# Kernel optimization log

Measured on AMD Instinct MI355X. Metric: run time of the kernel, lower is better.

Reference implementation:

```python
import jax, jax.numpy as jnp
import numpy as np

B, D, L, H = 512, 512, 32, 300  # batch, input_dim, latent_dim, hidden_dim


def setup_inputs() -> dict:
    key = jax.random.key(0)
    ks = jax.random.split(key, 16)
    s = lambda k, *sh: jax.random.normal(k, sh, dtype=jnp.float32) * 0.05
    return {
        "x": jax.random.normal(ks[0], (B, D), dtype=jnp.float32),
        "eps": jax.random.normal(ks[1], (B, L), dtype=jnp.float32),
        "W": jax.random.normal(ks[2], (D, L), dtype=jnp.float32),  # mask (get_generator_mask -> W)
        "qz_w1": s(ks[3], D, H), "qz_b1": s(ks[4], H),
        "qz_w2": s(ks[5], H, H), "qz_b2": s(ks[6], H),
        "zm_w": s(ks[7], H, L), "zm_b": s(ks[8], L),
        "zl_w": s(ks[9], H, L), "zl_b": s(ks[10], L),
        "gen_w1": s(ks[11], L, H),               # no bias (bias=False)
        "gen_w2": s(ks[12], H, H), "gen_b2": s(ks[13], H),
        "col_w": s(ks[14], D, H), "col_b": s(ks[15], D),  # stacked column_means Linears
    }


def reference(x, eps, W, qz_w1, qz_b1, qz_w2, qz_b2, zm_w, zm_b, zl_w, zl_b,
              gen_w1, gen_w2, gen_b2, col_w, col_b):
    # encode
    h = jax.nn.relu(x @ qz_w1 + qz_b1)
    h = jax.nn.relu(h @ qz_w2 + qz_b2)
    z_mean = h @ zm_w + zm_b
    z_log_var = h @ zl_w + zl_b
    # reparameterize (eps supplied as input)
    z = z_mean + eps * jnp.exp(0.5 * z_log_var)
    # decode: per-column masked generator MLP, batched over columns j
    masked = W[:, None, :] * z[None, :, :]                 # [D, B, L]
    g = jax.nn.relu(jnp.einsum('jbl,lh->jbh', masked, gen_w1))
    g = jax.nn.relu(jnp.einsum('jbh,hk->jbk', g, gen_w2) + gen_b2)
    x_rec = jnp.einsum('jbh,jh->jb', g, col_w) + col_b[:, None]  # [D, B]
    x_mean = x_rec.T                                       # [B, D]
    return (x_mean, z, z_mean, z_log_var)
```

## Files before the change

### kernel.cpp

```cpp
#include <hip/hip_runtime.h>

#define B_ 512
#define D_ 512
#define L_ 32
#define H_ 300
#define NT 19
#define NS 10
#define G1S 308

typedef unsigned short ushort_t;
typedef __bf16 bf16x8 __attribute__((ext_vector_type(8)));
typedef float f32x4 __attribute__((ext_vector_type(4)));

__device__ __forceinline__ float bf2f(unsigned int hi16) {
    return __uint_as_float(hi16 << 16);
}
__device__ __forceinline__ ushort_t f2bf(float f) {
    unsigned int u = __float_as_uint(f);
    u += 0x7fffu + ((u >> 16) & 1u);
    return (ushort_t)(u >> 16);
}

union B8 { ushort_t u[8]; uint4 q; bf16x8 v; uint2 d[2]; };

__global__ __launch_bounds__(64) void prep_kernel(
        const float* __restrict__ gw1, const float* __restrict__ gw2,
        const float* __restrict__ qw1, const float* __restrict__ qw2,
        const float* __restrict__ zmw, const float* __restrict__ zlw,
        ushort_t* __restrict__ gw1f, ushort_t* __restrict__ gw2f,
        ushort_t* __restrict__ w1hi, ushort_t* __restrict__ w1lo,
        ushort_t* __restrict__ w2hi, ushort_t* __restrict__ w2lo,
        ushort_t* __restrict__ w3hi, ushort_t* __restrict__ w3lo) {
    int blk = blockIdx.x;
    int l = threadIdx.x, grp = l >> 4, li = l & 15;
    if (blk < 209) {
        const float* src; int K, nt, s; ushort_t* dst;
        if (blk < 19) { nt = blk; s = 0; src = gw1; K = 32; dst = gw1f + (nt * 64 + l) * 8; }
        else { int i = blk - 19; nt = i / 10; s = i % 10; src = gw2; K = 300;
               dst = gw2f + ((nt * 10 + s) * 64 + l) * 8; }
        int n = nt * 16 + li;
        B8 V;
        #pragma unroll
        for (int i = 0; i < 8; ++i) {
            int k = 32 * s + 8 * grp + i;
            V.u[i] = f2bf((k < K && n < H_) ? src[k * H_ + n] : 0.f);
        }
        *reinterpret_cast<uint4*>(dst) = V.q;
    } else {
        const float* src = nullptr; int K, N, nt, s, stacked = 0;
        ushort_t *dh, *dl;
        if (blk < 513)      { int i = blk - 209; nt = i / 16; s = i % 16; src = qw1; K = 512; N = 300;
                              dh = w1hi + ((nt * 16 + s) * 64 + l) * 8; dl = w1lo + ((nt * 16 + s) * 64 + l) * 8; }
        else if (blk < 703) { int i = blk - 513; nt = i / 10; s = i % 10; src = qw2; K = 300; N = 300;
                              dh = w2hi + ((nt * 10 + s) * 64 + l) * 8; dl = w2lo + ((nt * 10 + s) * 64 + l) * 8; }
        else                { int i = blk - 703; nt = i / 10; s = i % 10; K = 300; N = 64; stacked = 1;
                              dh = w3hi + ((nt * 10 + s) * 64 + l) * 8; dl = w3lo + ((nt * 10 + s) * 64 + l) * 8; }
        int n = nt * 16 + li;
        B8 Vh, Vl;
        #pragma unroll
        for (int i = 0; i < 8; ++i) {
            int k = 32 * s + 8 * grp + i;
            float v = 0.f;
            if (k < K && n < N) {
                if (!stacked) v = src[k * N + n];
                else          v = (n < 32) ? zmw[k * 32 + n] : zlw[k * 32 + (n - 32)];
            }
            ushort_t h = f2bf(v);
            Vh.u[i] = h;
            Vl.u[i] = f2bf(v - bf2f(h));
        }
        *reinterpret_cast<uint4*>(dh) = Vh.q;
        *reinterpret_cast<uint4*>(dl) = Vl.q;
    }
}

template<int KSTEPS, bool RELU>
__global__ __launch_bounds__(256) void enc_gemm_f32(const float* __restrict__ A, int lda,
        const ushort_t* __restrict__ Whi, const ushort_t* __restrict__ Wlo,
        const float* __restrict__ bias, float* __restrict__ out, int ldo,
        int Ncols, int ntiles) {
    const int tid = threadIdx.x;
    const int w = tid >> 6, lane = tid & 63;
    const int grp = lane >> 4, li = lane & 15;
    const int r0 = blockIdx.x * 16;
    const int nt = blockIdx.y * 4 + w;
    const bool active = nt < ntiles;

    f32x4 acc = {0.f, 0.f, 0.f, 0.f};
    for (int s = 0; s < KSTEPS; ++s) {
        int kb = 32 * s + 8 * grp;
        B8 Ah, Al;
        if (kb + 8 <= lda) {
            const float* ap = A + (size_t)(r0 + li) * lda + kb;
            float4 f0 = *reinterpret_cast<const float4*>(ap);
            float4 f1 = *reinterpret_cast<const float4*>(ap + 4);
            float fv[8] = {f0.x, f0.y, f0.z, f0.w, f1.x, f1.y, f1.z, f1.w};
            #pragma unroll
            for (int i = 0; i < 8; ++i) {
                ushort_t h = f2bf(fv[i]);
                Ah.u[i] = h;
                Al.u[i] = f2bf(fv[i] - bf2f(h));
            }
        } else {
            Ah.q = make_uint4(0, 0, 0, 0);
            Al.q = make_uint4(0, 0, 0, 0);
        }
        if (active) {
            bf16x8 bh = *reinterpret_cast<const bf16x8*>(
                Whi + ((size_t)(nt * KSTEPS + s) * 64 + lane) * 8);
            bf16x8 bl = *reinterpret_cast<const bf16x8*>(
                Wlo + ((size_t)(nt * KSTEPS + s) * 64 + lane) * 8);
            acc = __builtin_amdgcn_mfma_f32_16x16x32_bf16(Ah.v, bh, acc, 0, 0, 0);
            acc = __builtin_amdgcn_mfma_f32_16x16x32_bf16(Al.v, bh, acc, 0, 0, 0);
            acc = __builtin_amdgcn_mfma_f32_16x16x32_bf16(Ah.v, bl, acc, 0, 0, 0);
        }
    }
    if (active) {
        int h = nt * 16 + li;
        float bv = (bias != nullptr && h < Ncols) ? bias[h] : 0.f;
        #pragma unroll
        for (int r = 0; r < 4; ++r) {
            float v = acc[r] + bv;
            if (RELU) v = fmaxf(v, 0.f);
            if (h >= Ncols) v = 0.f;
            out[(size_t)(r0 + 4 * grp + r) * ldo + h] = v;
        }
    }
}

__global__ __launch_bounds__(256) void enc3_reparam(const float* __restrict__ h2,
        const ushort_t* __restrict__ w3hi, const ushort_t* __restrict__ w3lo,
        const float* __restrict__ zmb, const float* __restrict__ zlb,
        const float* __restrict__ eps, float* __restrict__ out, float* __restrict__ zb) {
    __shared__ float zs[16][64];
    const int tid = threadIdx.x;
    const int w = tid >> 6, lane = tid & 63;
    const int grp = lane >> 4, li = lane & 15;
    const int r0 = blockIdx.x * 16;

    f32x4 acc = {0.f, 0.f, 0.f, 0.f};
    for (int s = 0; s < 10; ++s) {
        int kb = 32 * s + 8 * grp;
        B8 Ah, Al;
        if (kb + 8 <= 304) {
            const float* ap = h2 + (size_t)(r0 + li) * 304 + kb;
            float4 f0 = *reinterpret_cast<const float4*>(ap);
            float4 f1 = *reinterpret_cast<const float4*>(ap + 4);
            float fv[8] = {f0.x, f0.y, f0.z, f0.w, f1.x, f1.y, f1.z, f1.w};
            #pragma unroll
            for (int i = 0; i < 8; ++i) {
                ushort_t h = f2bf(fv[i]);
                Ah.u[i] = h;
                Al.u[i] = f2bf(fv[i] - bf2f(h));
            }
        } else {
            Ah.q = make_uint4(0, 0, 0, 0);
            Al.q = make_uint4(0, 0, 0, 0);
        }
        bf16x8 bh = *reinterpret_cast<const bf16x8*>(w3hi + ((size_t)(w * 10 + s) * 64 + lane) * 8);
        bf16x8 bl = *reinterpret_cast<const bf16x8*>(w3lo + ((size_t)(w * 10 + s) * 64 + lane) * 8);
        acc = __builtin_amdgcn_mfma_f32_16x16x32_bf16(Ah.v, bh, acc, 0, 0, 0);
        acc = __builtin_amdgcn_mfma_f32_16x16x32_bf16(Al.v, bh, acc, 0, 0, 0);
        acc = __builtin_amdgcn_mfma_f32_16x16x32_bf16(Ah.v, bl, acc, 0, 0, 0);
    }
    #pragma unroll
    for (int r = 0; r < 4; ++r) zs[4 * grp + r][w * 16 + li] = acc[r];
    __syncthreads();

    for (int idx = tid; idx < 512; idx += 256) {
        int m = idx >> 5, l2 = idx & 31;
        int row = r0 + m;
        float zm = zs[m][l2] + zmb[l2];
        float zl = zs[m][32 + l2] + zlb[l2];
        float zv = zm + eps[row * 32 + l2] * expf(0.5f * zl);
        out[B_ * D_ + row * 32 + l2] = zv;
        out[B_ * D_ + B_ * L_ + row * 32 + l2] = zm;
        out[B_ * D_ + 2 * B_ * L_ + row * 32 + l2] = zl;
        zb[row * 32 + l2] = zv;
    }
}

__global__ __launch_bounds__(512, 4) void decode_kernel(
        const float* __restrict__ z, const float* __restrict__ Wmask,
        const ushort_t* __restrict__ gw1f, const ushort_t* __restrict__ gw2f,
        const float* __restrict__ gb2, const float* __restrict__ colw,
        const float* __restrict__ colb, float* __restrict__ xmean) {
    __shared__ __align__(16) ushort_t g1s[64 * G1S + 16];
    __shared__ float xrec[64];

    const int j    = blockIdx.y;
    const int b0   = blockIdx.x * 64;
    const int tid  = threadIdx.x;
    const int w    = tid >> 6;
    const int lane = tid & 63;
    const int grp  = lane >> 4, li = lane & 15;
    const int ntl  = (w < 3) ? 3 : 2;

    B8 bm[4];
    {
        const float* wp = Wmask + (size_t)j * L_ + 8 * grp;
        float4 w0 = *reinterpret_cast<const float4*>(wp);
        float4 w1 = *reinterpret_cast<const float4*>(wp + 4);
        #pragma unroll
        for (int mt = 0; mt < 4; ++mt) {
            const float* zp = z + (size_t)(b0 + mt * 16 + li) * L_ + 8 * grp;
            float4 z0 = *reinterpret_cast<const float4*>(zp);
            float4 z1 = *reinterpret_cast<const float4*>(zp + 4);
            bm[mt].u[0] = f2bf(w0.x * z0.x); bm[mt].u[1] = f2bf(w0.y * z0.y);
            bm[mt].u[2] = f2bf(w0.z * z0.z); bm[mt].u[3] = f2bf(w0.w * z0.w);
            bm[mt].u[4] = f2bf(w1.x * z1.x); bm[mt].u[5] = f2bf(w1.y * z1.y);
            bm[mt].u[6] = f2bf(w1.z * z1.z); bm[mt].u[7] = f2bf(w1.w * z1.w);
        }
        if (tid < 64) xrec[tid] = 0.f;
        if (tid < 272) {
            if (tid < 256) g1s[(tid >> 2) * G1S + 304 + (tid & 3)] = 0;
            else           g1s[64 * G1S + (tid - 256)] = 0;
        }
    }
    __syncthreads();

    #pragma unroll
    for (int t = 0; t < 3; ++t) {
        if (t < ntl) {
            int nt = w + 8 * t;
            bf16x8 ga = *reinterpret_cast<const bf16x8*>(gw1f + (nt * 64 + lane) * 8);
            #pragma unroll
            for (int mt = 0; mt < 4; ++mt) {
                f32x4 c = {0.f, 0.f, 0.f, 0.f};
                c = __builtin_amdgcn_mfma_f32_16x16x32_bf16(bm[mt].v, ga, c, 0, 0, 0);
                #pragma unroll
                for (int r = 0; r < 4; ++r)
                    g1s[(mt * 16 + 4 * grp + r) * G1S + nt * 16 + li] =
                        f2bf(fmaxf(c[r], 0.f));
            }
        }
    }
    __syncthreads();

    {
        f32x4 acc[4][3];
        #pragma unroll
        for (int mt = 0; mt < 4; ++mt)
            #pragma unroll
            for (int t = 0; t < 3; ++t) acc[mt][t] = {0.f, 0.f, 0.f, 0.f};

        for (int s = 0; s < NS; ++s) {
            B8 af[4];
            #pragma unroll
            for (int mt = 0; mt < 4; ++mt) {
                const ushort_t* p = &g1s[(mt * 16 + li) * G1S + 32 * s + 8 * grp];
                af[mt].d[0] = *reinterpret_cast<const uint2*>(p);
                af[mt].d[1] = *reinterpret_cast<const uint2*>(p + 4);
            }
            #pragma unroll
            for (int t = 0; t < 3; ++t) {
                if (t < ntl) {
                    int nt = w + 8 * t;
                    bf16x8 bfr = *reinterpret_cast<const bf16x8*>(
                        gw2f + ((size_t)(nt * NS + s) * 64 + lane) * 8);
                    #pragma unroll
                    for (int mt = 0; mt < 4; ++mt)
                        acc[mt][t] = __builtin_amdgcn_mfma_f32_16x16x32_bf16(
                            af[mt].v, bfr, acc[mt][t], 0, 0, 0);
                }
            }
        }

        float partial[4][4] = {};
        #pragma unroll
        for (int t = 0; t < 3; ++t) {
            if (t < ntl) {
                int h = (w + 8 * t) * 16 + li;
                float bias = 0.f, fac = 0.f;
                if (h < H_) { bias = gb2[h]; fac = colw[j * H_ + h]; }
                #pragma unroll
                for (int mt = 0; mt < 4; ++mt)
                    #pragma unroll
                    for (int r = 0; r < 4; ++r)
                        partial[mt][r] += fmaxf(acc[mt][t][r] + bias, 0.f) * fac;
            }
        }
        #pragma unroll
        for (int mt = 0; mt < 4; ++mt)
            #pragma unroll
            for (int r = 0; r < 4; ++r) {
                float v = partial[mt][r];
                v += __shfl_xor(v, 1);
                v += __shfl_xor(v, 2);
                v += __shfl_xor(v, 4);
                v += __shfl_xor(v, 8);
                if (li == 0) atomicAdd(&xrec[mt * 16 + grp * 4 + r], v);
            }
    }
    __syncthreads();

    if (tid < 64) xmean[(size_t)(b0 + tid) * D_ + j] = xrec[tid] + colb[j];
}

extern "C" void kernel_launch(void* const* d_in, const int* in_sizes, int n_in,
                              void* d_out, int out_size, void* d_ws, size_t ws_size,
                              hipStream_t stream) {
    const float* x     = (const float*)d_in[0];
    const float* eps   = (const float*)d_in[1];
    const float* Wm    = (const float*)d_in[2];
    const float* qz_w1 = (const float*)d_in[3];
    const float* qz_b1 = (const float*)d_in[4];
    const float* qz_w2 = (const float*)d_in[5];
    const float* qz_b2 = (const float*)d_in[6];
    const float* zm_w  = (const float*)d_in[7];
    const float* zm_b  = (const float*)d_in[8];
    const float* zl_w  = (const float*)d_in[9];
    const float* zl_b  = (const float*)d_in[10];
    const float* gw1   = (const float*)d_in[11];
    const float* gw2   = (const float*)d_in[12];
    const float* gb2   = (const float*)d_in[13];
    const float* colw  = (const float*)d_in[14];
    const float* colb  = (const float*)d_in[15];
    float* out = (float*)d_out;
    char* ws = (char*)d_ws;

    ushort_t* gw1f = (ushort_t*)(ws + 0);
    ushort_t* gw2f = (ushort_t*)(ws + 19456);
    ushort_t* w1hi = (ushort_t*)(ws + 214016);
    ushort_t* w1lo = (ushort_t*)(ws + 525312);
    ushort_t* w2hi = (ushort_t*)(ws + 836608);
    ushort_t* w2lo = (ushort_t*)(ws + 1031168);
    ushort_t* w3hi = (ushort_t*)(ws + 1225728);
    ushort_t* w3lo = (ushort_t*)(ws + 1266688);
    float*    h1   = (float*)(ws + 1307648);
    float*    h2   = (float*)(ws + 214016);
    float*    zb   = (float*)(ws + 1930240);

    prep_kernel<<<743, 64, 0, stream>>>(gw1, gw2, qz_w1, qz_w2, zm_w, zl_w,
                                        gw1f, gw2f, w1hi, w1lo, w2hi, w2lo, w3hi, w3lo);
    enc_gemm_f32<16, true><<<dim3(32, 5), 256, 0, stream>>>(
        x, 512, w1hi, w1lo, qz_b1, h1, 304, 300, NT);
    enc_gemm_f32<10, true><<<dim3(32, 5), 256, 0, stream>>>(
        h1, 304, w2hi, w2lo, qz_b2, h2, 304, 300, NT);
    enc3_reparam<<<32, 256, 0, stream>>>(h2, w3hi, w3lo, zm_b, zl_b, eps, out, zb);
    decode_kernel<<<dim3(8, 512), 512, 0, stream>>>(zb, Wm, gw1f, gw2f, gb2, colw, colb, out);
}
```

Measured before the change: 136.6 us.

## Use native bf16 conversions, transposed first-layer MFMA, and per-wave partial sums

Replaces the hand-written round-to-nearest bf16 conversion with native __bf16 casts, which the compiler can lower to hardware conversion instructions. In the decoder, the first MFMA swaps its A and B operands so each lane writes four contiguous bf16 values with one 8-byte LDS store instead of four scattered 2-byte stores. The shared atomicAdd reduction is replaced with per-wave partial arrays summed by 64 threads, and the second GEMM loop is unrolled by 2. Several independent micro-optimisations are bundled, and the operand swap changes the accumulator layout that the g1s store indexing must match.

```diff
diff --git a/kernel.cpp b/kernel.cpp
--- a/kernel.cpp
+++ b/kernel.cpp
@@ -12,16 +12,16 @@
 typedef __bf16 bf16x8 __attribute__((ext_vector_type(8)));
 typedef float f32x4 __attribute__((ext_vector_type(4)));
 
-__device__ __forceinline__ float bf2f(unsigned int hi16) {
-    return __uint_as_float(hi16 << 16);
-}
-__device__ __forceinline__ ushort_t f2bf(float f) {
-    unsigned int u = __float_as_uint(f);
-    u += 0x7fffu + ((u >> 16) & 1u);
-    return (ushort_t)(u >> 16);
-}
-
-union B8 { ushort_t u[8]; uint4 q; bf16x8 v; uint2 d[2]; };
+union B8 { ushort_t u[8]; uint4 q; bf16x8 v; uint2 d[2]; __bf16 b[8]; };
+
+__device__ __forceinline__ void split8(const float* fv, B8& hi, B8& lo) {
+    #pragma unroll
+    for (int i = 0; i < 8; ++i) {
+        __bf16 h = (__bf16)fv[i];
+        hi.b[i] = h;
+        lo.b[i] = (__bf16)(fv[i] - (float)h);
+    }
+}
 
 __global__ __launch_bounds__(64) void prep_kernel(
         const float* __restrict__ gw1, const float* __restrict__ gw2,
@@ -43,7 +43,7 @@
         #pragma unroll
         for (int i = 0; i < 8; ++i) {
             int k = 32 * s + 8 * grp + i;
-            V.u[i] = f2bf((k < K && n < H_) ? src[k * H_ + n] : 0.f);
+            V.b[i] = (__bf16)((k < K && n < H_) ? src[k * H_ + n] : 0.f);
         }
         *reinterpret_cast<uint4*>(dst) = V.q;
     } else {
@@ -56,7 +56,7 @@
         else                { int i = blk - 703; nt = i / 10; s = i % 10; K = 300; N = 64; stacked = 1;
                               dh = w3hi + ((nt * 10 + s) * 64 + l) * 8; dl = w3lo + ((nt * 10 + s) * 64 + l) * 8; }
         int n = nt * 16 + li;
-        B8 Vh, Vl;
+        float fv[8];
         #pragma unroll
         for (int i = 0; i < 8; ++i) {
             int k = 32 * s + 8 * grp + i;
@@ -65,10 +65,10 @@
                 if (!stacked) v = src[k * N + n];
                 else          v = (n < 32) ? zmw[k * 32 + n] : zlw[k * 32 + (n - 32)];
             }
-            ushort_t h = f2bf(v);
-            Vh.u[i] = h;
-            Vl.u[i] = f2bf(v - bf2f(h));
-        }
+            fv[i] = v;
+        }
+        B8 Vh, Vl;
+        split8(fv, Vh, Vl);
         *reinterpret_cast<uint4*>(dh) = Vh.q;
         *reinterpret_cast<uint4*>(dl) = Vl.q;
     }
@@ -95,12 +95,7 @@
             float4 f0 = *reinterpret_cast<const float4*>(ap);
             float4 f1 = *reinterpret_cast<const float4*>(ap + 4);
             float fv[8] = {f0.x, f0.y, f0.z, f0.w, f1.x, f1.y, f1.z, f1.w};
-            #pragma unroll
-            for (int i = 0; i < 8; ++i) {
-                ushort_t h = f2bf(fv[i]);
-                Ah.u[i] = h;
-                Al.u[i] = f2bf(fv[i] - bf2f(h));
-            }
+            split8(fv, Ah, Al);
         } else {
             Ah.q = make_uint4(0, 0, 0, 0);
             Al.q = make_uint4(0, 0, 0, 0);
@@ -147,12 +142,7 @@
             float4 f0 = *reinterpret_cast<const float4*>(ap);
             float4 f1 = *reinterpret_cast<const float4*>(ap + 4);
             float fv[8] = {f0.x, f0.y, f0.z, f0.w, f1.x, f1.y, f1.z, f1.w};
-            #pragma unroll
-            for (int i = 0; i < 8; ++i) {
-                ushort_t h = f2bf(fv[i]);
-                Ah.u[i] = h;
-                Al.u[i] = f2bf(fv[i] - bf2f(h));
-            }
+            split8(fv, Ah, Al);
         } else {
             Ah.q = make_uint4(0, 0, 0, 0);
             Al.q = make_uint4(0, 0, 0, 0);
@@ -186,7 +176,7 @@
         const float* __restrict__ gb2, const float* __restrict__ colw,
         const float* __restrict__ colb, float* __restrict__ xmean) {
     __shared__ __align__(16) ushort_t g1s[64 * G1S + 16];
-    __shared__ float xrec[64];
+    __shared__ float xpart[8][64];
 
     const int j    = blockIdx.y;
     const int b0   = blockIdx.x * 64;
@@ -201,17 +191,16 @@
         const float* wp = Wmask + (size_t)j * L_ + 8 * grp;
         float4 w0 = *reinterpret_cast<const float4*>(wp);
         float4 w1 = *reinterpret_cast<const float4*>(wp + 4);
+        float wv[8] = {w0.x, w0.y, w0.z, w0.w, w1.x, w1.y, w1.z, w1.w};
         #pragma unroll
         for (int mt = 0; mt < 4; ++mt) {
             const float* zp = z + (size_t)(b0 + mt * 16 + li) * L_ + 8 * grp;
             float4 z0 = *reinterpret_cast<const float4*>(zp);
             float4 z1 = *reinterpret_cast<const float4*>(zp + 4);
-            bm[mt].u[0] = f2bf(w0.x * z0.x); bm[mt].u[1] = f2bf(w0.y * z0.y);
-            bm[mt].u[2] = f2bf(w0.z * z0.z); bm[mt].u[3] = f2bf(w0.w * z0.w);
-            bm[mt].u[4] = f2bf(w1.x * z1.x); bm[mt].u[5] = f2bf(w1.y * z1.y);
-            bm[mt].u[6] = f2bf(w1.z * z1.z); bm[mt].u[7] = f2bf(w1.w * z1.w);
-        }
-        if (tid < 64) xrec[tid] = 0.f;
+            float zv[8] = {z0.x, z0.y, z0.z, z0.w, z1.x, z1.y, z1.z, z1.w};
+            #pragma unroll
+            for (int i = 0; i < 8; ++i) bm[mt].b[i] = (__bf16)(wv[i] * zv[i]);
+        }
         if (tid < 272) {
             if (tid < 256) g1s[(tid >> 2) * G1S + 304 + (tid & 3)] = 0;
             else           g1s[64 * G1S + (tid - 256)] = 0;
@@ -227,11 +216,11 @@
             #pragma unroll
             for (int mt = 0; mt < 4; ++mt) {
                 f32x4 c = {0.f, 0.f, 0.f, 0.f};
-                c = __builtin_amdgcn_mfma_f32_16x16x32_bf16(bm[mt].v, ga, c, 0, 0, 0);
+                c = __builtin_amdgcn_mfma_f32_16x16x32_bf16(ga, bm[mt].v, c, 0, 0, 0);
+                B8 P;
                 #pragma unroll
-                for (int r = 0; r < 4; ++r)
-                    g1s[(mt * 16 + 4 * grp + r) * G1S + nt * 16 + li] =
-                        f2bf(fmaxf(c[r], 0.f));
+                for (int r = 0; r < 4; ++r) P.b[r] = (__bf16)fmaxf(c[r], 0.f);
+                *reinterpret_cast<uint2*>(&g1s[(mt * 16 + li) * G1S + nt * 16 + 4 * grp]) = P.d[0];
             }
         }
     }
@@ -244,6 +233,7 @@
             #pragma unroll
             for (int t = 0; t < 3; ++t) acc[mt][t] = {0.f, 0.f, 0.f, 0.f};
 
+        #pragma unroll 2
         for (int s = 0; s < NS; ++s) {
             B8 af[4];
             #pragma unroll
@@ -289,12 +279,17 @@
                 v += __shfl_xor(v, 2);
                 v += __shfl_xor(v, 4);
                 v += __shfl_xor(v, 8);
-                if (li == 0) atomicAdd(&xrec[mt * 16 + grp * 4 + r], v);
+                if (li == 0) xpart[w][mt * 16 + 4 * grp + r] = v;
             }
     }
     __syncthreads();
 
-    if (tid < 64) xmean[(size_t)(b0 + tid) * D_ + j] = xrec[tid] + colb[j];
+    if (tid < 64) {
+        float v = colb[j];
+        #pragma unroll
+        for (int ww = 0; ww < 8; ++ww) v += xpart[ww][tid];
+        xmean[(size_t)(b0 + tid) * D_ + j] = v;
+    }
 }
 
 extern "C" void kernel_launch(void* const* d_in, const int* in_sizes, int n_in,
```

Result: faster. 127.2 us (-6.9%).
